# Performance work log

Measured on AMD Instinct MI355X. Metric: run time of the kernel, lower is better.

The kernel has to match this reference:

```python
import jax, jax.numpy as jnp
import numpy as np

N_USERS = 100000
N_ITEMS = 50000
N_NODES = N_USERS + N_ITEMS
EMB_DIM = 64
N_EDGES = 1200000
N_LAYERS = 3


def setup_inputs() -> dict:
    key = jax.random.key(0)
    k1, k2, k3, k4, k5 = jax.random.split(key, 5)
    edge_row = jax.random.randint(k1, (N_EDGES,), 0, N_NODES, dtype=jnp.int32)
    edge_col = jax.random.randint(k2, (N_EDGES,), 0, N_NODES, dtype=jnp.int32)
    edge_weight = jax.random.uniform(k3, (N_EDGES,), dtype=jnp.float32)
    # xavier_uniform for nn.Embedding: bound = sqrt(6/(fan_in+fan_out))
    bu = float(np.sqrt(6.0 / (N_USERS + EMB_DIM)))
    bi = float(np.sqrt(6.0 / (N_ITEMS + EMB_DIM)))
    user_emb = jax.random.uniform(k4, (N_USERS, EMB_DIM), jnp.float32, -bu, bu)
    item_emb = jax.random.uniform(k5, (N_ITEMS, EMB_DIM), jnp.float32, -bi, bi)
    return {
        "edge_row": edge_row,
        "edge_col": edge_col,
        "edge_weight": edge_weight,
        "user_emb": user_emb,
        "item_emb": item_emb,
    }


def _spmm(edge_row, edge_col, edge_weight, x):
    # y[i] = sum_{e: row[e]==i} w[e] * x[col[e]]  (COO sparse @ dense)
    gathered = x[edge_col] * edge_weight[:, None]  # [E, d]
    return jax.ops.segment_sum(gathered, edge_row, num_segments=N_NODES)


def reference(edge_row, edge_col, edge_weight, user_emb, item_emb):
    x = jnp.concatenate([user_emb, item_emb], axis=0)  # [N, d]
    acc = x  # running sum over layer outputs (layer 0 = initial embeddings)
    for _ in range(N_LAYERS):
        x = _spmm(edge_row, edge_col, edge_weight, x)
        acc = acc + x
    mean_emb = acc / (N_LAYERS + 1)
    return mean_emb[:N_USERS], mean_emb[N_USERS:]
```

## Files before the change

### kernel.cpp

```cpp
#include <hip/hip_runtime.h>
#include <hip/hip_bf16.h>


#define EMB 64
#define BUCKET_SHIFT 9
#define BROWS (1 << BUCKET_SHIFT)
#define NBUCK_PAD 320
#define S1_CHUNK 2048
#define BCAP 4608
#define S2_CAP 12
#define SPMM_BLOCKS 2048

typedef _Float16 h8 __attribute__((ext_vector_type(8)));
typedef _Float16 h2v __attribute__((ext_vector_type(2)));
typedef float f2v __attribute__((ext_vector_type(2)));
typedef float f4 __attribute__((ext_vector_type(4)));
typedef int i2v __attribute__((ext_vector_type(2)));

union H8U { h8 v; h2v p[4]; };

__global__ void s1_convert(const int* __restrict__ row, const int* __restrict__ col,
                           const float* __restrict__ w, int* __restrict__ cursor1,
                           int2* __restrict__ tmp,
                           const float* __restrict__ ue, const float* __restrict__ ie,
                           h8* __restrict__ X0h, int nu_elems, int total8,
                           int E, int s1Blocks) {
    int t = threadIdx.x;
    if ((int)blockIdx.x < s1Blocks) {
        __shared__ int lcount[NBUCK_PAD];
        __shared__ int lbase[NBUCK_PAD];
        int c0 = blockIdx.x * S1_CHUNK;
        if (t < NBUCK_PAD) lcount[t] = 0;
        __syncthreads();
        int pkc[S1_CHUNK / 512];
        int cc[S1_CHUNK / 512];
        int rr[S1_CHUNK / 512];
        float ww[S1_CHUNK / 512];
        #pragma unroll
        for (int i = 0; i < S1_CHUNK / 512; i++) {
            int e = c0 + i * 512 + t;
            pkc[i] = -1;
            if (e < E) {
                int r = row[e];
                int b = r >> BUCKET_SHIFT;
                int rank = atomicAdd(&lcount[b], 1);
                pkc[i] = (b << 12) | rank;
                cc[i] = col[e];
                rr[i] = r & (BROWS - 1);
                ww[i] = w[e];
            }
        }
        __syncthreads();
        if (t < NBUCK_PAD) {
            int c = lcount[t];
            if (c) lbase[t] = atomicAdd(&cursor1[t], c);
        }
        __syncthreads();
        #pragma unroll
        for (int i = 0; i < S1_CHUNK / 512; i++) {
            if (pkc[i] >= 0) {
                int b = pkc[i] >> 12;
                int pos = lbase[b] + (pkc[i] & 4095);
                if (pos < BCAP)
                    tmp[(size_t)b * BCAP + pos] =
                        make_int2((cc[i] << BUCKET_SHIFT) | rr[i], __float_as_int(ww[i]));
            }
        }
    } else {
        int g = (blockIdx.x - s1Blocks) * 512 + t;
        if (g >= total8) return;
        int base = g << 3;
        const f4* src = (const f4*)((base < nu_elems) ? (ue + base)
                                                      : (ie + (base - nu_elems)));
        f4 a = src[0], b = src[1];
        h8 o;
        o[0] = (_Float16)a.x; o[1] = (_Float16)a.y; o[2] = (_Float16)a.z; o[3] = (_Float16)a.w;
        o[4] = (_Float16)b.x; o[5] = (_Float16)b.y; o[6] = (_Float16)b.z; o[7] = (_Float16)b.w;
        X0h[g] = o;
    }
}

__global__ void scatter2(const int* __restrict__ cursor1, const int2* __restrict__ tmp,
                         int2* __restrict__ cw, int* __restrict__ rbeg,
                         int* __restrict__ rend, int nrows) {
    __shared__ int cnt[BROWS];
    __shared__ int wS[8];
    int t = threadIdx.x;
    int j = blockIdx.x;
    int rowbase = j << BUCKET_SHIFT;
    int rows_here = nrows - rowbase;
    if (rows_here > BROWS) rows_here = BROWS;
    int num = cursor1[j];
    if (num > BCAP) num = BCAP;
    int base = j * BCAP;
    int iters = (num + 511) >> 9;

    cnt[t] = 0;
    __syncthreads();

    int pkc[S2_CAP];
    int rk[S2_CAP];
    int wv[S2_CAP];
    bool cached = (iters <= S2_CAP);
    if (cached) {
        for (int i = 0; i < iters; i++) {
            int p = i * 512 + t;
            pkc[i] = -1;
            if (p < num) {
                int2 rec = tmp[base + p];
                pkc[i] = rec.x;
                wv[i] = rec.y;
                rk[i] = atomicAdd(&cnt[rec.x & (BROWS - 1)], 1);
            }
        }
    } else {
        for (int p = t; p < num; p += 512)
            atomicAdd(&cnt[tmp[base + p].x & (BROWS - 1)], 1);
    }
    __syncthreads();

    int v = cnt[t];
    int lane = t & 63;
    int wave = t >> 6;
    int s = v;
    #pragma unroll
    for (int off = 1; off < 64; off <<= 1) {
        int tt = __shfl_up(s, off, 64);
        if (lane >= off) s += tt;
    }
    if (lane == 63) wS[wave] = s;
    __syncthreads();
    int woff = 0;
    for (int w = 0; w < wave; w++) woff += wS[w];
    int excl = woff + s - v;
    if (t < rows_here) {
        rbeg[rowbase + t] = base + excl;
        rend[rowbase + t] = base + excl + v;
    }
    __syncthreads();
    cnt[t] = excl;
    __syncthreads();

    if (cached) {
        for (int i = 0; i < iters; i++) {
            if (pkc[i] >= 0) {
                int r = pkc[i] & (BROWS - 1);
                cw[base + cnt[r] + rk[i]] = make_int2(pkc[i] >> BUCKET_SHIFT, wv[i]);
            }
        }
    } else {
        for (int p = t; p < num; p += 512) {
            int2 rec = tmp[base + p];
            int r = rec.x & (BROWS - 1);
            int pos = atomicAdd(&cnt[r], 1);
            cw[base + pos] = make_int2(rec.x >> BUCKET_SHIFT, rec.y);
        }
    }
}

template <bool LAST>
__global__ __launch_bounds__(256) void spmm_kernel(
        const int* __restrict__ rbeg, const int* __restrict__ rend,
        const i2v* __restrict__ cw,
        const h8* __restrict__ Xin, h8* __restrict__ Xout,
        const h8* __restrict__ X0, const h8* __restrict__ X1,
        float* __restrict__ out, int nrows) {
    int lane = threadIdx.x & 63;
    int g = lane >> 3;
    int l8 = lane & 7;
    int wv = (blockIdx.x * blockDim.x + threadIdx.x) >> 6;
    int totWaves = (gridDim.x * blockDim.x) >> 6;

    for (int base8 = wv * 8; base8 < nrows; base8 += totWaves * 8) {
        int row = base8 + g;
        bool valid = row < nrows;
        int beg = valid ? rbeg[row] : 0;
        int end = valid ? rend[row] : 0;

        f2v acc2[4];
        #pragma unroll
        for (int k = 0; k < 4; k++) acc2[k] = (f2v){0.f, 0.f};

        int e = beg;
        for (; e + 1 < end; e += 2) {
            i2v c0 = cw[e];
            i2v c1 = cw[e + 1];
            H8U v0, v1;
            v0.v = Xin[(c0.x << 3) + l8];
            v1.v = Xin[(c1.x << 3) + l8];
            float w0 = __int_as_float(c0.y);
            float w1 = __int_as_float(c1.y);
            f2v w0p = (f2v){w0, w0};
            f2v w1p = (f2v){w1, w1};
            #pragma unroll
            for (int k = 0; k < 4; k++) {
                acc2[k] += w0p * __builtin_convertvector(v0.p[k], f2v);
                acc2[k] += w1p * __builtin_convertvector(v1.p[k], f2v);
            }
        }
        if (e < end) {
            i2v c0 = cw[e];
            H8U v0;
            v0.v = Xin[(c0.x << 3) + l8];
            float w0 = __int_as_float(c0.y);
            f2v w0p = (f2v){w0, w0};
            #pragma unroll
            for (int k = 0; k < 4; k++)
                acc2[k] += w0p * __builtin_convertvector(v0.p[k], f2v);
        }

        float* a = (float*)acc2;
        if (valid) {
            if (LAST) {
                h8 x0 = X0[(row << 3) + l8];
                h8 v1 = X1[(row << 3) + l8];
                h8 v2 = Xin[(row << 3) + l8];
                int base = (row << 6) + (l8 << 3);
                f4 o0, o1;
                o0.x = 0.25f * ((float)x0[0] + (float)v1[0] + (float)v2[0] + a[0]);
                o0.y = 0.25f * ((float)x0[1] + (float)v1[1] + (float)v2[1] + a[1]);
                o0.z = 0.25f * ((float)x0[2] + (float)v1[2] + (float)v2[2] + a[2]);
                o0.w = 0.25f * ((float)x0[3] + (float)v1[3] + (float)v2[3] + a[3]);
                o1.x = 0.25f * ((float)x0[4] + (float)v1[4] + (float)v2[4] + a[4]);
                o1.y = 0.25f * ((float)x0[5] + (float)v1[5] + (float)v2[5] + a[5]);
                o1.z = 0.25f * ((float)x0[6] + (float)v1[6] + (float)v2[6] + a[6]);
                o1.w = 0.25f * ((float)x0[7] + (float)v1[7] + (float)v2[7] + a[7]);
                f4* dst = (f4*)(out + base);
                dst[0] = o0;
                dst[1] = o1;
            } else {
                h8 o;
                #pragma unroll
                for (int k = 0; k < 8; k++) o[k] = (_Float16)a[k];
                Xout[(row << 3) + l8] = o;
            }
        }
    }
}

extern "C" void kernel_launch(void* const* d_in, const int* in_sizes, int n_in,
                              void* d_out, int out_size, void* d_ws, size_t ws_size,
                              hipStream_t stream) {
    const int* edge_row = (const int*)d_in[0];
    const int* edge_col = (const int*)d_in[1];
    const float* edge_w = (const float*)d_in[2];
    const float* user_emb = (const float*)d_in[3];
    const float* item_emb = (const float*)d_in[4];

    const int E = in_sizes[0];
    const int nu_elems = in_sizes[3];
    const int ni_elems = in_sizes[4];
    const int total = nu_elems + ni_elems;
    const int N = total / EMB;
    const int NBUCK = (N + BROWS - 1) >> BUCKET_SHIFT;

    size_t off = 0;
    auto carve = [&](size_t bytes) {
        void* p = (char*)d_ws + off;
        off += (bytes + 255) & ~(size_t)255;
        return p;
    };
    h8*    X0h     = (h8*)carve((size_t)total * 2);
    h8*    X1h     = (h8*)carve((size_t)total * 2);
    h8*    X2h     = (h8*)carve((size_t)total * 2);
    int*   rbeg    = (int*)carve((size_t)N * 4);
    int*   rend    = (int*)carve((size_t)N * 4);
    int*   cursor1 = (int*)carve((size_t)NBUCK * 4);
    int2*  tmp     = (int2*)carve((size_t)NBUCK * BCAP * 8);
    int2*  cw      = (int2*)carve((size_t)NBUCK * BCAP * 8);
    (void)ws_size;

    float* out = (float*)d_out;

    const int total8 = total / 8;
    const int s1Blocks = (E + S1_CHUNK - 1) / S1_CHUNK;
    const int convBlocks = (total8 + 511) / 512;

    hipMemsetAsync(cursor1, 0, (size_t)NBUCK * 4, stream);
    s1_convert<<<s1Blocks + convBlocks, 512, 0, stream>>>(
        edge_row, edge_col, edge_w, cursor1, tmp,
        user_emb, item_emb, X0h, nu_elems, total8, E, s1Blocks);
    scatter2<<<NBUCK, 512, 0, stream>>>(cursor1, tmp, cw, rbeg, rend, N);

    spmm_kernel<false><<<SPMM_BLOCKS, 256, 0, stream>>>(rbeg, rend, (const i2v*)cw,
                                                        X0h, X1h, nullptr, nullptr,
                                                        nullptr, N);
    spmm_kernel<false><<<SPMM_BLOCKS, 256, 0, stream>>>(rbeg, rend, (const i2v*)cw,
                                                        X1h, X2h, nullptr, nullptr,
                                                        nullptr, N);
    spmm_kernel<true><<<SPMM_BLOCKS, 256, 0, stream>>>(rbeg, rend, (const i2v*)cw,
                                                       X2h, nullptr, X0h, X1h,
                                                       out, N);
}
```

Baseline: 229.4 us.

## Sort rows by degree within each bucket to balance SpMM wave work

The scatter kernel builds a per-bucket histogram of row degrees and emits a permutation that groups rows of similar degree together. The SpMM kernels read rows through this permutation, so the 8 rows a wave handles at once have similar edge counts and fewer lanes sit idle. The cost is an extra indirection load per row, writes that are no longer contiguous in row order, and a little more work in the scatter kernel.

```diff
diff --git a/kernel.cpp b/kernel.cpp
--- a/kernel.cpp
+++ b/kernel.cpp
@@ -82,9 +82,10 @@
 
 __global__ void scatter2(const int* __restrict__ cursor1, const int2* __restrict__ tmp,
                          int2* __restrict__ cw, int* __restrict__ rbeg,
-                         int* __restrict__ rend, int nrows) {
+                         int* __restrict__ rend, int* __restrict__ perm, int nrows) {
     __shared__ int cnt[BROWS];
     __shared__ int wS[8];
+    __shared__ int dh[64];
     int t = threadIdx.x;
     int j = blockIdx.x;
     int rowbase = j << BUCKET_SHIFT;
@@ -100,7 +101,7 @@
 
     int pkc[S2_CAP];
     int rk[S2_CAP];
-    int wv[S2_CAP];
+    int wvv[S2_CAP];
     bool cached = (iters <= S2_CAP);
     if (cached) {
         for (int i = 0; i < iters; i++) {
@@ -109,7 +110,7 @@
             if (p < num) {
                 int2 rec = tmp[base + p];
                 pkc[i] = rec.x;
-                wv[i] = rec.y;
+                wvv[i] = rec.y;
                 rk[i] = atomicAdd(&cnt[rec.x & (BROWS - 1)], 1);
             }
         }
@@ -139,13 +140,17 @@
     }
     __syncthreads();
     cnt[t] = excl;
-    __syncthreads();
+    if (t < 64) dh[t] = 0;
+    __syncthreads();
+
+    int bin = v < 63 ? v : 63;
+    if (t < rows_here) atomicAdd(&dh[bin], 1);
 
     if (cached) {
         for (int i = 0; i < iters; i++) {
             if (pkc[i] >= 0) {
                 int r = pkc[i] & (BROWS - 1);
-                cw[base + cnt[r] + rk[i]] = make_int2(pkc[i] >> BUCKET_SHIFT, wv[i]);
+                cw[base + cnt[r] + rk[i]] = make_int2(pkc[i] >> BUCKET_SHIFT, wvv[i]);
             }
         }
     } else {
@@ -156,10 +161,29 @@
             cw[base + pos] = make_int2(rec.x >> BUCKET_SHIFT, rec.y);
         }
     }
+    __syncthreads();
+
+    if (t < 64) {
+        int c = dh[t];
+        int ss = c;
+        #pragma unroll
+        for (int off = 1; off < 64; off <<= 1) {
+            int tt = __shfl_up(ss, off, 64);
+            if (t >= off) ss += tt;
+        }
+        dh[t] = ss - c;
+    }
+    __syncthreads();
+
+    if (t < rows_here) {
+        int pos = atomicAdd(&dh[bin], 1);
+        perm[rowbase + pos] = rowbase + t;
+    }
 }
 
 template <bool LAST>
 __global__ __launch_bounds__(256) void spmm_kernel(
+        const int* __restrict__ perm,
         const int* __restrict__ rbeg, const int* __restrict__ rend,
         const i2v* __restrict__ cw,
         const h8* __restrict__ Xin, h8* __restrict__ Xout,
@@ -172,8 +196,9 @@
     int totWaves = (gridDim.x * blockDim.x) >> 6;
 
     for (int base8 = wv * 8; base8 < nrows; base8 += totWaves * 8) {
-        int row = base8 + g;
-        bool valid = row < nrows;
+        int idx = base8 + g;
+        bool valid = idx < nrows;
+        int row = valid ? perm[idx] : 0;
         int beg = valid ? rbeg[row] : 0;
         int end = valid ? rend[row] : 0;
 
@@ -265,6 +290,7 @@
     h8*    X2h     = (h8*)carve((size_t)total * 2);
     int*   rbeg    = (int*)carve((size_t)N * 4);
     int*   rend    = (int*)carve((size_t)N * 4);
+    int*   perm    = (int*)carve((size_t)N * 4);
     int*   cursor1 = (int*)carve((size_t)NBUCK * 4);
     int2*  tmp     = (int2*)carve((size_t)NBUCK * BCAP * 8);
     int2*  cw      = (int2*)carve((size_t)NBUCK * BCAP * 8);
@@ -280,15 +306,15 @@
     s1_convert<<<s1Blocks + convBlocks, 512, 0, stream>>>(
         edge_row, edge_col, edge_w, cursor1, tmp,
         user_emb, item_emb, X0h, nu_elems, total8, E, s1Blocks);
-    scatter2<<<NBUCK, 512, 0, stream>>>(cursor1, tmp, cw, rbeg, rend, N);
-
-    spmm_kernel<false><<<SPMM_BLOCKS, 256, 0, stream>>>(rbeg, rend, (const i2v*)cw,
+    scatter2<<<NBUCK, 512, 0, stream>>>(cursor1, tmp, cw, rbeg, rend, perm, N);
+
+    spmm_kernel<false><<<SPMM_BLOCKS, 256, 0, stream>>>(perm, rbeg, rend, (const i2v*)cw,
                                                         X0h, X1h, nullptr, nullptr,
                                                         nullptr, N);
-    spmm_kernel<false><<<SPMM_BLOCKS, 256, 0, stream>>>(rbeg, rend, (const i2v*)cw,
+    spmm_kernel<false><<<SPMM_BLOCKS, 256, 0, stream>>>(perm, rbeg, rend, (const i2v*)cw,
                                                         X1h, X2h, nullptr, nullptr,
                                                         nullptr, N);
-    spmm_kernel<true><<<SPMM_BLOCKS, 256, 0, stream>>>(rbeg, rend, (const i2v*)cw,
+    spmm_kernel<true><<<SPMM_BLOCKS, 256, 0, stream>>>(perm, rbeg, rend, (const i2v*)cw,
                                                        X2h, nullptr, X0h, X1h,
                                                        out, N);
 }
```

Result: slower. 260.3 us (+13.5%).

## Fuse all stages into one cooperative persistent kernel with grid syncs

Applied to the files above, without the earlier changes.

Replaces the memset, bucketing/convert, scatter and three SpMM launches with a single cooperative kernel that separates the phases with grid-wide syncs. This removes per-launch overhead and the gaps between kernels. In exchange it adds grid-sync cost, shrinks blocks to 256 threads with grid-stride loops over the bucketing and scatter phases, and drops the register-cached scatter path. It also sizes the grid from an occupancy query that assumes 256 CUs.

```diff
diff --git a/kernel.cpp b/kernel.cpp
--- a/kernel.cpp
+++ b/kernel.cpp
@@ -1,15 +1,16 @@
 #include <hip/hip_runtime.h>
 #include <hip/hip_bf16.h>
+#include <hip/hip_cooperative_groups.h>
+
+namespace cg = cooperative_groups;
 
 
 #define EMB 64
 #define BUCKET_SHIFT 9
 #define BROWS (1 << BUCKET_SHIFT)
 #define NBUCK_PAD 320
-#define S1_CHUNK 2048
+#define CHUNK 1024
 #define BCAP 4608
-#define S2_CAP 12
-#define SPMM_BLOCKS 2048
 
 typedef _Float16 h8 __attribute__((ext_vector_type(8)));
 typedef _Float16 h2v __attribute__((ext_vector_type(2)));
@@ -19,158 +20,14 @@
 
 union H8U { h8 v; h2v p[4]; };
 
-__global__ void s1_convert(const int* __restrict__ row, const int* __restrict__ col,
-                           const float* __restrict__ w, int* __restrict__ cursor1,
-                           int2* __restrict__ tmp,
-                           const float* __restrict__ ue, const float* __restrict__ ie,
-                           h8* __restrict__ X0h, int nu_elems, int total8,
-                           int E, int s1Blocks) {
-    int t = threadIdx.x;
-    if ((int)blockIdx.x < s1Blocks) {
-        __shared__ int lcount[NBUCK_PAD];
-        __shared__ int lbase[NBUCK_PAD];
-        int c0 = blockIdx.x * S1_CHUNK;
-        if (t < NBUCK_PAD) lcount[t] = 0;
-        __syncthreads();
-        int pkc[S1_CHUNK / 512];
-        int cc[S1_CHUNK / 512];
-        int rr[S1_CHUNK / 512];
-        float ww[S1_CHUNK / 512];
-        #pragma unroll
-        for (int i = 0; i < S1_CHUNK / 512; i++) {
-            int e = c0 + i * 512 + t;
-            pkc[i] = -1;
-            if (e < E) {
-                int r = row[e];
-                int b = r >> BUCKET_SHIFT;
-                int rank = atomicAdd(&lcount[b], 1);
-                pkc[i] = (b << 12) | rank;
-                cc[i] = col[e];
-                rr[i] = r & (BROWS - 1);
-                ww[i] = w[e];
-            }
-        }
-        __syncthreads();
-        if (t < NBUCK_PAD) {
-            int c = lcount[t];
-            if (c) lbase[t] = atomicAdd(&cursor1[t], c);
-        }
-        __syncthreads();
-        #pragma unroll
-        for (int i = 0; i < S1_CHUNK / 512; i++) {
-            if (pkc[i] >= 0) {
-                int b = pkc[i] >> 12;
-                int pos = lbase[b] + (pkc[i] & 4095);
-                if (pos < BCAP)
-                    tmp[(size_t)b * BCAP + pos] =
-                        make_int2((cc[i] << BUCKET_SHIFT) | rr[i], __float_as_int(ww[i]));
-            }
-        }
-    } else {
-        int g = (blockIdx.x - s1Blocks) * 512 + t;
-        if (g >= total8) return;
-        int base = g << 3;
-        const f4* src = (const f4*)((base < nu_elems) ? (ue + base)
-                                                      : (ie + (base - nu_elems)));
-        f4 a = src[0], b = src[1];
-        h8 o;
-        o[0] = (_Float16)a.x; o[1] = (_Float16)a.y; o[2] = (_Float16)a.z; o[3] = (_Float16)a.w;
-        o[4] = (_Float16)b.x; o[5] = (_Float16)b.y; o[6] = (_Float16)b.z; o[7] = (_Float16)b.w;
-        X0h[g] = o;
-    }
-}
-
-__global__ void scatter2(const int* __restrict__ cursor1, const int2* __restrict__ tmp,
-                         int2* __restrict__ cw, int* __restrict__ rbeg,
-                         int* __restrict__ rend, int nrows) {
-    __shared__ int cnt[BROWS];
-    __shared__ int wS[8];
-    int t = threadIdx.x;
-    int j = blockIdx.x;
-    int rowbase = j << BUCKET_SHIFT;
-    int rows_here = nrows - rowbase;
-    if (rows_here > BROWS) rows_here = BROWS;
-    int num = cursor1[j];
-    if (num > BCAP) num = BCAP;
-    int base = j * BCAP;
-    int iters = (num + 511) >> 9;
-
-    cnt[t] = 0;
-    __syncthreads();
-
-    int pkc[S2_CAP];
-    int rk[S2_CAP];
-    int wv[S2_CAP];
-    bool cached = (iters <= S2_CAP);
-    if (cached) {
-        for (int i = 0; i < iters; i++) {
-            int p = i * 512 + t;
-            pkc[i] = -1;
-            if (p < num) {
-                int2 rec = tmp[base + p];
-                pkc[i] = rec.x;
-                wv[i] = rec.y;
-                rk[i] = atomicAdd(&cnt[rec.x & (BROWS - 1)], 1);
-            }
-        }
-    } else {
-        for (int p = t; p < num; p += 512)
-            atomicAdd(&cnt[tmp[base + p].x & (BROWS - 1)], 1);
-    }
-    __syncthreads();
-
-    int v = cnt[t];
-    int lane = t & 63;
-    int wave = t >> 6;
-    int s = v;
-    #pragma unroll
-    for (int off = 1; off < 64; off <<= 1) {
-        int tt = __shfl_up(s, off, 64);
-        if (lane >= off) s += tt;
-    }
-    if (lane == 63) wS[wave] = s;
-    __syncthreads();
-    int woff = 0;
-    for (int w = 0; w < wave; w++) woff += wS[w];
-    int excl = woff + s - v;
-    if (t < rows_here) {
-        rbeg[rowbase + t] = base + excl;
-        rend[rowbase + t] = base + excl + v;
-    }
-    __syncthreads();
-    cnt[t] = excl;
-    __syncthreads();
-
-    if (cached) {
-        for (int i = 0; i < iters; i++) {
-            if (pkc[i] >= 0) {
-                int r = pkc[i] & (BROWS - 1);
-                cw[base + cnt[r] + rk[i]] = make_int2(pkc[i] >> BUCKET_SHIFT, wv[i]);
-            }
-        }
-    } else {
-        for (int p = t; p < num; p += 512) {
-            int2 rec = tmp[base + p];
-            int r = rec.x & (BROWS - 1);
-            int pos = atomicAdd(&cnt[r], 1);
-            cw[base + pos] = make_int2(rec.x >> BUCKET_SHIFT, rec.y);
-        }
-    }
-}
-
 template <bool LAST>
-__global__ __launch_bounds__(256) void spmm_kernel(
+__device__ __forceinline__ void spmm_layer(
         const int* __restrict__ rbeg, const int* __restrict__ rend,
         const i2v* __restrict__ cw,
         const h8* __restrict__ Xin, h8* __restrict__ Xout,
         const h8* __restrict__ X0, const h8* __restrict__ X1,
-        float* __restrict__ out, int nrows) {
-    int lane = threadIdx.x & 63;
-    int g = lane >> 3;
-    int l8 = lane & 7;
-    int wv = (blockIdx.x * blockDim.x + threadIdx.x) >> 6;
-    int totWaves = (gridDim.x * blockDim.x) >> 6;
-
+        float* __restrict__ out, int nrows,
+        int wv, int totWaves, int g, int l8) {
     for (int base8 = wv * 8; base8 < nrows; base8 += totWaves * 8) {
         int row = base8 + g;
         bool valid = row < nrows;
@@ -238,6 +95,140 @@
     }
 }
 
+__global__ void __launch_bounds__(256) mega(
+        const int* __restrict__ row, const int* __restrict__ col,
+        const float* __restrict__ w, int* __restrict__ cursor1,
+        int2* __restrict__ tmp,
+        const float* __restrict__ ue, const float* __restrict__ ie,
+        h8* __restrict__ X0h, h8* __restrict__ X1h, h8* __restrict__ X2h,
+        int* __restrict__ rbeg, int* __restrict__ rend, int2* __restrict__ cw,
+        float* __restrict__ out,
+        int nu_elems, int total8, int E, int nrows, int nbuck) {
+    cg::grid_group grid = cg::this_grid();
+    __shared__ int lcount[NBUCK_PAD];
+    __shared__ int lbase[NBUCK_PAD];
+    __shared__ int cnt[BROWS];
+    int t = threadIdx.x;
+
+    if (blockIdx.x == 0)
+        for (int j = t; j < nbuck; j += 256) cursor1[j] = 0;
+    grid.sync();
+
+    int nChunks = (E + CHUNK - 1) / CHUNK;
+    for (int ch = blockIdx.x; ch < nChunks; ch += gridDim.x) {
+        int c0 = ch * CHUNK;
+        for (int j = t; j < NBUCK_PAD; j += 256) lcount[j] = 0;
+        __syncthreads();
+        int pkc[4], cc[4], rr[4];
+        float ww[4];
+        #pragma unroll
+        for (int i = 0; i < 4; i++) {
+            int e = c0 + i * 256 + t;
+            pkc[i] = -1;
+            if (e < E) {
+                int r = row[e];
+                int b = r >> BUCKET_SHIFT;
+                int rank = atomicAdd(&lcount[b], 1);
+                pkc[i] = (b << 12) | rank;
+                cc[i] = col[e];
+                rr[i] = r & (BROWS - 1);
+                ww[i] = w[e];
+            }
+        }
+        __syncthreads();
+        for (int j = t; j < NBUCK_PAD; j += 256) {
+            int c = lcount[j];
+            if (c) lbase[j] = atomicAdd(&cursor1[j], c);
+        }
+        __syncthreads();
+        #pragma unroll
+        for (int i = 0; i < 4; i++) {
+            if (pkc[i] >= 0) {
+                int b = pkc[i] >> 12;
+                int pos = lbase[b] + (pkc[i] & 4095);
+                if (pos < BCAP)
+                    tmp[(size_t)b * BCAP + pos] =
+                        make_int2((cc[i] << BUCKET_SHIFT) | rr[i], __float_as_int(ww[i]));
+            }
+        }
+        __syncthreads();
+    }
+    for (int g = blockIdx.x * 256 + t; g < total8; g += gridDim.x * 256) {
+        int base = g << 3;
+        const f4* src = (const f4*)((base < nu_elems) ? (ue + base)
+                                                      : (ie + (base - nu_elems)));
+        f4 a = src[0], b = src[1];
+        h8 o;
+        o[0] = (_Float16)a.x; o[1] = (_Float16)a.y; o[2] = (_Float16)a.z; o[3] = (_Float16)a.w;
+        o[4] = (_Float16)b.x; o[5] = (_Float16)b.y; o[6] = (_Float16)b.z; o[7] = (_Float16)b.w;
+        X0h[g] = o;
+    }
+    grid.sync();
+
+    if ((int)blockIdx.x < nbuck) {
+        int j = blockIdx.x;
+        int rowbase = j << BUCKET_SHIFT;
+        int rows_here = nrows - rowbase;
+        if (rows_here > BROWS) rows_here = BROWS;
+        int num = cursor1[j];
+        if (num > BCAP) num = BCAP;
+        int base = j * BCAP;
+
+        cnt[t] = 0;
+        cnt[t + 256] = 0;
+        __syncthreads();
+        for (int p = t; p < num; p += 256)
+            atomicAdd(&cnt[tmp[base + p].x & (BROWS - 1)], 1);
+        __syncthreads();
+
+        int k0 = t << 1, k1 = k0 | 1;
+        int c0 = cnt[k0], c1 = cnt[k1];
+        int psum = c0 + c1;
+        int lane = t & 63;
+        int wave = t >> 6;
+        int s = psum;
+        #pragma unroll
+        for (int off = 1; off < 64; off <<= 1) {
+            int tt = __shfl_up(s, off, 64);
+            if (lane >= off) s += tt;
+        }
+        if (lane == 63) lbase[wave] = s;
+        __syncthreads();
+        int woff = 0;
+        for (int wv2 = 0; wv2 < wave; wv2++) woff += lbase[wv2];
+        int e0 = woff + s - psum;
+        int e1 = e0 + c0;
+        if (k0 < rows_here) { rbeg[rowbase + k0] = base + e0; rend[rowbase + k0] = base + e0 + c0; }
+        if (k1 < rows_here) { rbeg[rowbase + k1] = base + e1; rend[rowbase + k1] = base + e1 + c1; }
+        cnt[k0] = e0;
+        cnt[k1] = e1;
+        __syncthreads();
+
+        for (int p = t; p < num; p += 256) {
+            int2 rec = tmp[base + p];
+            int r = rec.x & (BROWS - 1);
+            int pos = atomicAdd(&cnt[r], 1);
+            cw[base + pos] = make_int2(rec.x >> BUCKET_SHIFT, rec.y);
+        }
+    }
+    grid.sync();
+
+    int lane = t & 63;
+    int g8 = lane >> 3;
+    int l8 = lane & 7;
+    int wv = (blockIdx.x * blockDim.x + t) >> 6;
+    int totWaves = (gridDim.x * blockDim.x) >> 6;
+
+    spmm_layer<false>(rbeg, rend, (const i2v*)cw, X0h, X1h, nullptr, nullptr,
+                      nullptr, nrows, wv, totWaves, g8, l8);
+    grid.sync();
+    spmm_layer<false>(rbeg, rend, (const i2v*)cw, X1h, X2h, nullptr, nullptr,
+                      nullptr, nrows, wv, totWaves, g8, l8);
+    grid.sync();
+    spmm_layer<true>(rbeg, rend, (const i2v*)cw, X2h, nullptr, X0h, X1h,
+                     out, nrows, wv, totWaves, g8, l8);
+}
+
 extern "C" void kernel_launch(void* const* d_in, const int* in_sizes, int n_in,
                               void* d_out, int out_size, void* d_ws, size_t ws_size,
                               hipStream_t stream) {
@@ -251,8 +242,8 @@
     const int nu_elems = in_sizes[3];
     const int ni_elems = in_sizes[4];
     const int total = nu_elems + ni_elems;
-    const int N = total / EMB;
-    const int NBUCK = (N + BROWS - 1) >> BUCKET_SHIFT;
+    int N = total / EMB;
+    int NBUCK = (N + BROWS - 1) >> BUCKET_SHIFT;
 
     size_t off = 0;
     auto carve = [&](size_t bytes) {
@@ -271,24 +262,22 @@
     (void)ws_size;
 
     float* out = (float*)d_out;
-
-    const int total8 = total / 8;
-    const int s1Blocks = (E + S1_CHUNK - 1) / S1_CHUNK;
-    const int convBlocks = (total8 + 511) / 512;
-
-    hipMemsetAsync(cursor1, 0, (size_t)NBUCK * 4, stream);
-    s1_convert<<<s1Blocks + convBlocks, 512, 0, stream>>>(
-        edge_row, edge_col, edge_w, cursor1, tmp,
-        user_emb, item_emb, X0h, nu_elems, total8, E, s1Blocks);
-    scatter2<<<NBUCK, 512, 0, stream>>>(cursor1, tmp, cw, rbeg, rend, N);
-
-    spmm_kernel<false><<<SPMM_BLOCKS, 256, 0, stream>>>(rbeg, rend, (const i2v*)cw,
-                                                        X0h, X1h, nullptr, nullptr,
-                                                        nullptr, N);
-    spmm_kernel<false><<<SPMM_BLOCKS, 256, 0, stream>>>(rbeg, rend, (const i2v*)cw,
-                                                        X1h, X2h, nullptr, nullptr,
-                                                        nullptr, N);
-    spmm_kernel<true><<<SPMM_BLOCKS, 256, 0, stream>>>(rbeg, rend, (const i2v*)cw,
-                                                       X2h, nullptr, X0h, X1h,
-                                                       out, N);
+    int total8 = total / 8;
+
+    int occ = 0;
+    hipError_t oe = hipOccupancyMaxActiveBlocksPerMultiprocessor(&occ, mega, 256, 0);
+    if (oe != hipSuccess || occ <= 0) occ = 4;
+    int grid = occ * 256;
+    if (grid > 2048) grid = 2048;
+
+    void* args[] = {
+        (void*)&edge_row, (void*)&edge_col, (void*)&edge_w,
+        (void*)&cursor1, (void*)&tmp,
+        (void*)&user_emb, (void*)&item_emb,
+        (void*)&X0h, (void*)&X1h, (void*)&X2h,
+        (void*)&rbeg, (void*)&rend, (void*)&cw,
+        (void*)&out,
+        (void*)&nu_elems, (void*)&total8, (void*)&E, (void*)&N, (void*)&NBUCK,
+    };
+    hipLaunchCooperativeKernel((void*)mega, dim3(grid), dim3(256), args, 0, stream);
 }
```

Result: slower. 916.9 us (+299.8%).
